# Kernel optimization log

Measured on AMD Instinct MI355X. Metric: run time of the kernel, lower is better.

Reference implementation:

```python
import jax, jax.numpy as jnp
import numpy as np

DIM = 512
N_GROUPS = 8
N_CODES = 1024
SUB = DIM // N_GROUPS
CB_LAMBDA = 1.0
COMMIT_LAMBDA = 0.25


def setup_inputs() -> dict:
    key = jax.random.key(0)
    k1, k2, k3 = jax.random.split(key, 3)
    x = jax.random.normal(k1, (8, DIM, 4096), dtype=jnp.float32)
    lim = 1.0 / N_CODES
    codebooks1 = jax.random.uniform(k2, (N_GROUPS, N_CODES, SUB), dtype=jnp.float32, minval=-lim, maxval=lim)
    codebooks2 = jax.random.uniform(k3, (N_GROUPS, N_CODES, SUB), dtype=jnp.float32, minval=-lim, maxval=lim)
    return {"x": x, "codebooks1": codebooks1, "codebooks2": codebooks2}


def _quantize_group(flat, cbs):
    # flat: (N, G, d), cbs: (G, K, d)
    x2 = jnp.sum(flat * flat, axis=-1, keepdims=True)          # (N, G, 1)
    e2 = jnp.sum(cbs * cbs, axis=-1)                            # (G, K)
    xe = jnp.einsum('ngd,gkd->ngk', flat, cbs)                  # (N, G, K)
    d = x2 + e2[None, :, :] - 2.0 * xe                          # (N, G, K)
    idx = jnp.argmin(d, axis=-1)                                # (N, G)
    z = cbs[jnp.arange(N_GROUPS)[None, :], idx]                 # (N, G, d)
    return z, idx


def reference(x, codebooks1, codebooks2):
    B, C, T = x.shape
    sg = jax.lax.stop_gradient
    # (B, C, T) -> (B*T, G, sub)
    xb = jnp.transpose(x, (0, 2, 1)).reshape(-1, N_GROUPS, SUB)
    residual = xb
    quantized = jnp.zeros_like(xb)
    losses = []
    all_indices = []
    for cbs in (codebooks1, codebooks2):
        z, idx = _quantize_group(residual, cbs)
        codebook_loss = jnp.mean((z - sg(residual)) ** 2)
        commit_loss = jnp.mean((sg(z) - residual) ** 2)
        losses.append(CB_LAMBDA * codebook_loss + COMMIT_LAMBDA * commit_loss)
        z_st = residual + sg(z - residual)  # straight-through
        residual = residual - z_st
        quantized = quantized + z_st
        all_indices.append(idx)
    total_loss = jnp.mean(jnp.stack(losses))
    quantized_out = jnp.transpose(quantized.reshape(B, T, C), (0, 2, 1))
    # indices in original order: layer-major, group-major -> (layers*G, B*T)
    indices = jnp.concatenate([idx.T for idx in all_indices], axis=0)
    return quantized_out, total_loss, indices
```

## Files before the change

kernel.cpp:

```cpp
#include <hip/hip_runtime.h>

#define GRP 8
#define SUBD 64
#define NCODE 1024
#define TLEN 4096
#define NBATCH 8
#define NVEC (NBATCH * TLEN)
#define QOUT (NBATCH * 512 * TLEN)
#define ROWS 128
#define NGRPS (NCODE / 8)

#define WS_E2   64
#define WS_IDX1 (WS_E2 + 65536)
#define WS_P1   (WS_IDX1 + 1048576)
#define WS_P2   (WS_P1 + 2097152)

typedef const __attribute__((address_space(1))) char GCHAR;
typedef __attribute__((address_space(3))) char LCHAR;

__global__ __launch_bounds__(256) void k_e2(const float* __restrict__ cb1,
                                            const float* __restrict__ cb2,
                                            float* __restrict__ e2) {
    int i = blockIdx.x * 256 + threadIdx.x;
    const float* c = (i < GRP * NCODE) ? (cb1 + (size_t)i * SUBD)
                                       : (cb2 + (size_t)(i - GRP * NCODE) * SUBD);
    float s = 0.f;
#pragma unroll
    for (int d = 0; d < SUBD; ++d) s = __builtin_fmaf(c[d], c[d], s);
    e2[i] = s;
}

__global__ __launch_bounds__(256) void k_panel(const float* __restrict__ cb1,
                                               const float* __restrict__ cb2,
                                               float* __restrict__ cbP1,
                                               float* __restrict__ cbP2) {
    int i = blockIdx.x * 256 + threadIdx.x;
    int sel = i >> 13, rest = i & 8191, g = rest >> 10, k = rest & 1023;
    int grp = k >> 3, j = k & 7;
    const float* src = (sel ? cb2 : cb1) + ((size_t)g * NCODE + k) * SUBD;
    float* dst = (sel ? cbP2 : cbP1) + ((size_t)(g * NGRPS + grp) * SUBD) * 8 + j;
#pragma unroll
    for (int s = 0; s < 16; ++s) {
        float4 v = ((const float4*)src)[s];
#pragma unroll
        for (int dd = 0; dd < 4; ++dd) dst[(4 * s + dd) * 8] = ((const float*)&v)[dd];
    }
}

template <int STAGE2>
__global__ __launch_bounds__(256, 4) void k_vq(
    const float* __restrict__ x,
    const float* __restrict__ cb1,
    const float* __restrict__ cb2,
    const float* __restrict__ cbP,
    const float* __restrict__ e2,
    const int* __restrict__ idxPrev,
    int* __restrict__ idxOut,
    float* __restrict__ outIdxF,
    float* __restrict__ qout,
    double* __restrict__ lossAcc)
{
    __shared__ __align__(16) float xs[SUBD * ROWS];
    __shared__ float bdH[2 * ROWS];
    __shared__ int   biH[2 * ROWS];
    __shared__ int   i2s[ROWS];
    __shared__ double wsr[8];

    const int tid = threadIdx.x, w = tid >> 6, lane = tid & 63;
    const int g = blockIdx.y;
    const int row0 = blockIdx.x * ROWS;
    const int bz = row0 / TLEN, t0 = row0 % TLEN;
    const float* xsrc = x + ((size_t)(bz * 512 + g * SUBD)) * TLEN + t0;

    {
#pragma unroll
        for (int q = 0; q < 8; ++q) {
            int inst = w * 8 + q;
            int d = inst * 2 + (lane >> 5);
            const float* gp = xsrc + (size_t)d * TLEN + (lane & 31) * 4;
            float* lp = xs + inst * 256;
            __builtin_amdgcn_global_load_lds((GCHAR*)gp, (LCHAR*)lp, 16, 0, 0);
        }
    }
    __syncthreads();

    const int rowB = tid & 127, hi = tid >> 7;
    double ls1 = 0.0;
    int i1 = 0;
    if (STAGE2) {
        i1 = idxPrev[g * NVEC + row0 + rowB];
        const float4* z1v = (const float4*)(cb1 + ((size_t)g * NCODE + i1) * SUBD) + hi * 8;
#pragma unroll
        for (int s = 0; s < 8; ++s) {
            float4 z = z1v[s];
#pragma unroll
            for (int dd = 0; dd < 4; ++dd) {
                int d = hi * 32 + s * 4 + dd;
                float r = xs[d * ROWS + rowB];
                float zz = (&z.x)[dd];
                float tt = zz - r;
                float zst = r + tt;
                ls1 += (double)(tt * tt);
                float r2 = r - zst;
                xs[d * ROWS + rowB] = r2;
            }
        }
        __syncthreads();
    }

    const int w_u = __builtin_amdgcn_readfirstlane(w);
    const int half = w_u & 1;
    const int row = (w_u >> 1) * 64 + lane;

    float x2 = 0.f;
#pragma unroll 8
    for (int d = 0; d < SUBD; ++d) {
        float r = xs[d * ROWS + row];
        x2 = __builtin_fmaf(r, r, x2);
    }

    const float* cph = cbP + (size_t)g * (NGRPS * SUBD * 8) + (size_t)(half * 64) * (SUBD * 8);
    const float* e2h = e2 + g * NCODE + half * 512;

    float best = 1e30f;
    int bidx = 0;
    for (int ib = 0; ib < 16; ++ib) {
        const float* cp = cph + ib * 4 * (SUBD * 8);
        float acc[4][8];
#pragma unroll
        for (int gg = 0; gg < 4; ++gg)
#pragma unroll
            for (int j = 0; j < 8; ++j) acc[gg][j] = 0.f;

#pragma unroll 4
        for (int d = 0; d < SUBD; ++d) {
            float xv = xs[d * ROWS + row];
#pragma unroll
            for (int gg = 0; gg < 4; ++gg) {
                const float* cb8 = cp + gg * (SUBD * 8) + d * 8;
#pragma unroll
                for (int j = 0; j < 8; ++j)
                    acc[gg][j] = __builtin_fmaf(xv, cb8[j], acc[gg][j]);
            }
        }

#pragma unroll
        for (int gg = 0; gg < 4; ++gg) {
            const float* ep = e2h + (ib * 4 + gg) * 8;
#pragma unroll
            for (int j = 0; j < 8; ++j) {
                int k = half * 512 + (ib * 4 + gg) * 8 + j;
                float tv = x2 + ep[j];
                float dist = __builtin_fmaf(-2.0f, acc[gg][j], tv);
                if (dist < best) { best = dist; bidx = k; }
            }
        }
    }
    bdH[half * ROWS + row] = best;
    biH[half * ROWS + row] = bidx;
    __syncthreads();

    if (!(w_u & 1)) {
        float d0 = bdH[row];
        int   k0 = biH[row];
        float d1 = bdH[ROWS + row];
        int   k1 = biH[ROWS + row];
        int bi = (d1 < d0) ? k1 : k0;
        int nv = row0 + row;
        outIdxF[(size_t)g * NVEC + nv] = (float)bi;
        if (!STAGE2) idxOut[g * NVEC + nv] = bi;
        else i2s[row] = bi;
    }

    double ls2 = 0.0;
    if (STAGE2) {
        __syncthreads();
        int bi = i2s[rowB];
        const float4* z1v = (const float4*)(cb1 + ((size_t)g * NCODE + i1) * SUBD) + hi * 8;
        const float4* z2v = (const float4*)(cb2 + ((size_t)g * NCODE + bi) * SUBD) + hi * 8;
        const float* xp = xsrc + rowB;
        float* op = qout + ((size_t)(bz * 512 + g * SUBD)) * TLEN + t0 + rowB;
#pragma unroll
        for (int s = 0; s < 8; ++s) {
            float4 z1 = z1v[s];
            float4 z2 = z2v[s];
#pragma unroll
            for (int dd = 0; dd < 4; ++dd) {
                int d = hi * 32 + s * 4 + dd;
                float xv = xp[(size_t)d * TLEN];
                float r2 = xs[d * ROWS + rowB];
                float z1f = (&z1.x)[dd];
                float z2f = (&z2.x)[dd];
                float t1 = z1f - xv;
                float zst1 = xv + t1;
                float t2 = z2f - r2;
                float zst2 = r2 + t2;
                float qv = zst1 + zst2;
                op[(size_t)d * TLEN] = qv;
                ls2 += (double)(t2 * t2);
            }
        }

#pragma unroll
        for (int off = 32; off; off >>= 1) {
            ls1 += __shfl_down(ls1, off, 64);
            ls2 += __shfl_down(ls2, off, 64);
        }
        if (lane == 0) { wsr[w] = ls1; wsr[4 + w] = ls2; }
        __syncthreads();
        if (tid == 0)
            atomicAdd(lossAcc + 0, wsr[0] + wsr[1] + wsr[2] + wsr[3]);
        else if (tid == 64)
            atomicAdd(lossAcc + 1, wsr[4] + wsr[5] + wsr[6] + wsr[7]);
    }
}

__global__ void k_final(float* __restrict__ lossOut, const double* __restrict__ lossAcc) {
    double m = (lossAcc[0] + lossAcc[1]) / (double)QOUT;
    lossOut[0] = (float)(0.625 * m);
}

extern "C" void kernel_launch(void* const* d_in, const int* in_sizes, int n_in,
                              void* d_out, int out_size, void* d_ws, size_t ws_size,
                              hipStream_t stream) {
    const float* x   = (const float*)d_in[0];
    const float* cb1 = (const float*)d_in[1];
    const float* cb2 = (const float*)d_in[2];
    float* out = (float*)d_out;

    char* ws = (char*)d_ws;
    double* lossAcc = (double*)ws;
    float* e2   = (float*)(ws + WS_E2);
    int*   idx1 = (int*)(ws + WS_IDX1);
    float* cbP1 = (float*)(ws + WS_P1);
    float* cbP2 = (float*)(ws + WS_P2);

    hipMemsetAsync(ws, 0, 16, stream);

    k_e2<<<dim3(64), dim3(256), 0, stream>>>(cb1, cb2, e2);
    k_panel<<<dim3(64), dim3(256), 0, stream>>>(cb1, cb2, cbP1, cbP2);

    dim3 grid(NVEC / ROWS, GRP);
    float* outIdx = out + QOUT + 1;
    k_vq<0><<<grid, dim3(256), 0, stream>>>(x, cb1, cb2, cbP1, e2,
                                            nullptr, idx1, outIdx, nullptr, nullptr);
    k_vq<1><<<grid, dim3(256), 0, stream>>>(x, cb1, cb2, cbP2, e2 + GRP * NCODE,
                                            idx1, nullptr, outIdx + (size_t)GRP * NVEC,
                                            out, lossAcc);
    k_final<<<1, 1, 0, stream>>>(out + QOUT, lossAcc);
}
```

Baseline: 921.8 us.

## Register-block two rows per thread and split codebook across four waves

Each wave now handles all 128 rows (two per lane) against a quarter of the codebook, so every codebook value loaded is reused for two FMAs instead of one. The previous split (two row-halves by two codebook halves) is replaced by a four-way codebook split with a four-way argmin reduction in shared memory. Accumulators double to 64 registers, so launch bounds drop to two blocks per SIMD, which lowers occupancy in exchange for halved codebook load traffic per FMA.

```diff
diff --git a/kernel.cpp b/kernel.cpp
--- a/kernel.cpp
+++ b/kernel.cpp
@@ -48,7 +48,7 @@
 }
 
 template <int STAGE2>
-__global__ __launch_bounds__(256, 4) void k_vq(
+__global__ __launch_bounds__(256, 2) void k_vq(
     const float* __restrict__ x,
     const float* __restrict__ cb1,
     const float* __restrict__ cb2,
@@ -61,8 +61,8 @@
     double* __restrict__ lossAcc)
 {
     __shared__ __align__(16) float xs[SUBD * ROWS];
-    __shared__ float bdH[2 * ROWS];
-    __shared__ int   biH[2 * ROWS];
+    __shared__ float bdH[4 * ROWS];
+    __shared__ int   biH[4 * ROWS];
     __shared__ int   i2s[ROWS];
     __shared__ double wsr[8];
 
@@ -109,67 +109,80 @@
     }
 
     const int w_u = __builtin_amdgcn_readfirstlane(w);
-    const int half = w_u & 1;
-    const int row = (w_u >> 1) * 64 + lane;
-
-    float x2 = 0.f;
+
+    float x2a = 0.f, x2b = 0.f;
 #pragma unroll 8
     for (int d = 0; d < SUBD; ++d) {
-        float r = xs[d * ROWS + row];
-        x2 = __builtin_fmaf(r, r, x2);
-    }
-
-    const float* cph = cbP + (size_t)g * (NGRPS * SUBD * 8) + (size_t)(half * 64) * (SUBD * 8);
-    const float* e2h = e2 + g * NCODE + half * 512;
-
-    float best = 1e30f;
-    int bidx = 0;
-    for (int ib = 0; ib < 16; ++ib) {
-        const float* cp = cph + ib * 4 * (SUBD * 8);
-        float acc[4][8];
-#pragma unroll
-        for (int gg = 0; gg < 4; ++gg)
-#pragma unroll
-            for (int j = 0; j < 8; ++j) acc[gg][j] = 0.f;
-
-#pragma unroll 4
+        float ra = xs[d * ROWS + lane];
+        float rb = xs[d * ROWS + 64 + lane];
+        x2a = __builtin_fmaf(ra, ra, x2a);
+        x2b = __builtin_fmaf(rb, rb, x2b);
+    }
+
+    const float* e2g = e2 + g * NCODE;
+    float best[2] = {1e30f, 1e30f};
+    int bidx[2] = {0, 0};
+
+    for (int ib = 0; ib < 8; ++ib) {
+        const float* cp = cbP + ((size_t)(g * NGRPS) + w_u * 32 + ib * 4) * (SUBD * 8);
+        float acc[2][4][8];
+#pragma unroll
+        for (int r = 0; r < 2; ++r)
+#pragma unroll
+            for (int gg = 0; gg < 4; ++gg)
+#pragma unroll
+                for (int j = 0; j < 8; ++j) acc[r][gg][j] = 0.f;
+
+#pragma unroll 2
         for (int d = 0; d < SUBD; ++d) {
-            float xv = xs[d * ROWS + row];
+            float xa = xs[d * ROWS + lane];
+            float xb = xs[d * ROWS + 64 + lane];
 #pragma unroll
             for (int gg = 0; gg < 4; ++gg) {
-                const float* cb8 = cp + gg * (SUBD * 8) + d * 8;
-#pragma unroll
-                for (int j = 0; j < 8; ++j)
-                    acc[gg][j] = __builtin_fmaf(xv, cb8[j], acc[gg][j]);
+                const float* c8 = cp + gg * (SUBD * 8) + d * 8;
+#pragma unroll
+                for (int j = 0; j < 8; ++j) {
+                    float cv = c8[j];
+                    acc[0][gg][j] = __builtin_fmaf(xa, cv, acc[0][gg][j]);
+                    acc[1][gg][j] = __builtin_fmaf(xb, cv, acc[1][gg][j]);
+                }
             }
         }
 
 #pragma unroll
         for (int gg = 0; gg < 4; ++gg) {
-            const float* ep = e2h + (ib * 4 + gg) * 8;
 #pragma unroll
             for (int j = 0; j < 8; ++j) {
-                int k = half * 512 + (ib * 4 + gg) * 8 + j;
-                float tv = x2 + ep[j];
-                float dist = __builtin_fmaf(-2.0f, acc[gg][j], tv);
-                if (dist < best) { best = dist; bidx = k; }
-            }
-        }
-    }
-    bdH[half * ROWS + row] = best;
-    biH[half * ROWS + row] = bidx;
+                int k = w_u * 256 + ib * 32 + gg * 8 + j;
+                float ev = e2g[k];
+                float tva = x2a + ev;
+                float da = __builtin_fmaf(-2.0f, acc[0][gg][j], tva);
+                if (da < best[0]) { best[0] = da; bidx[0] = k; }
+                float tvb = x2b + ev;
+                float db = __builtin_fmaf(-2.0f, acc[1][gg][j], tvb);
+                if (db < best[1]) { best[1] = db; bidx[1] = k; }
+            }
+        }
+    }
+    bdH[w * ROWS + lane]      = best[0];
+    biH[w * ROWS + lane]      = bidx[0];
+    bdH[w * ROWS + 64 + lane] = best[1];
+    biH[w * ROWS + 64 + lane] = bidx[1];
     __syncthreads();
 
-    if (!(w_u & 1)) {
-        float d0 = bdH[row];
-        int   k0 = biH[row];
-        float d1 = bdH[ROWS + row];
-        int   k1 = biH[ROWS + row];
-        int bi = (d1 < d0) ? k1 : k0;
-        int nv = row0 + row;
+    if (tid < ROWS) {
+        float bd = bdH[tid];
+        int   bi = biH[tid];
+#pragma unroll
+        for (int wv = 1; wv < 4; ++wv) {
+            float od = bdH[wv * ROWS + tid];
+            int   oi = biH[wv * ROWS + tid];
+            if (od < bd) { bd = od; bi = oi; }
+        }
+        int nv = row0 + tid;
         outIdxF[(size_t)g * NVEC + nv] = (float)bi;
         if (!STAGE2) idxOut[g * NVEC + nv] = bi;
-        else i2s[row] = bi;
+        else i2s[tid] = bi;
     }
 
     double ls2 = 0.0;
```

Result: no change. 930.5 us (+0.9%).
